# Optimization experiments

Hardware: AMD Instinct MI355X
Metric: run time of the kernel (lower is better)

Reference implementation:

```python
import jax, jax.numpy as jnp
import numpy as np

N_NODES = 100000
N_EDGES = 1250000
D_FEAT = 64
K = 10          # propagation steps (hardcoded in module)
ALPHA = 0.1     # teleport probability (hardcoded in module)


def setup_inputs() -> dict:
    key = jax.random.key(0)
    k1, k2 = jax.random.split(key)
    x = jax.random.normal(k1, (N_NODES, D_FEAT), dtype=jnp.float32)
    # edge_index[0] = source nodes (j), edge_index[1] = target nodes (i)
    edge_index = jax.random.randint(k2, (2, N_EDGES), 0, N_NODES, dtype=jnp.int32)
    return {"x": x, "edge_index": edge_index}


def reference(x, edge_index):
    # PyG APPNP with add_self_loops=False, dropout=0:
    #   gcn_norm: deg[i] = sum of unit edge weights into i (scatter on col)
    #   norm_e = deg^{-1/2}[row_e] * deg^{-1/2}[col_e]
    #   h_{k+1} = (1 - alpha) * A_hat h_k + alpha * x
    row, col = edge_index[0], edge_index[1]
    ones = jnp.ones((edge_index.shape[1],), dtype=x.dtype)
    deg = jax.ops.segment_sum(ones, col, num_segments=N_NODES)
    dinv_sqrt = jnp.where(deg > 0, jax.lax.rsqrt(jnp.where(deg > 0, deg, 1.0)), 0.0)
    norm = dinv_sqrt[row] * dinv_sqrt[col]  # [E]

    h = x
    for _ in range(K):
        # gather-scale-scatter: messages norm_e * h[src_e], aggregated at dst_e
        msg = norm[:, None] * h[row]                           # [E, D]
        agg = jax.ops.segment_sum(msg, col, num_segments=N_NODES)  # [N, D]
        h = (1.0 - ALPHA) * agg + ALPHA * x
    return h
```

## Files before the change

kernel.cpp:

```cpp
#include <hip/hip_runtime.h>

constexpr int DFEAT  = 64;
constexpr int KSTEPS = 10;
constexpr float ALPHA = 0.1f;
constexpr int PAD    = 4;

constexpr int SCAN_T    = 256;
constexpr int SCAN_I    = 4;
constexpr int SCAN_TILE = SCAN_T * SCAN_I;

typedef unsigned int u32;
typedef __attribute__((ext_vector_type(4))) unsigned int u32x4;

__device__ inline u32 f2bf(float f) {
    u32 u = __float_as_uint(f);
    return ((u + 0x7fffu + ((u >> 16) & 1u)) >> 16) & 0xFFFFu;
}
__device__ inline float bfLO(u32 v) { return __uint_as_float(v << 16); }
__device__ inline float bfHI(u32 v) { return __uint_as_float(v & 0xFFFF0000u); }

__global__ void k_hist(const int* __restrict__ col, int* __restrict__ deg, int E) {
    int stride = gridDim.x * blockDim.x;
    for (int e = blockIdx.x * blockDim.x + threadIdx.x; e < E; e += stride)
        atomicAdd(&deg[col[e]], 1);
}

__global__ void k_dinv(const int* __restrict__ deg, float* __restrict__ dinv,
                       int* __restrict__ dpad, int N) {
    int stride = gridDim.x * blockDim.x;
    for (int i = blockIdx.x * blockDim.x + threadIdx.x; i < N; i += stride) {
        int d = deg[i];
        dinv[i] = (d > 0) ? rsqrtf((float)d) : 0.0f;
        dpad[i] = (d + (PAD - 1)) & ~(PAD - 1);
    }
}

__global__ void k_scan1(const int* __restrict__ in, int* __restrict__ out,
                        int* __restrict__ bsum, int n) {
    __shared__ int s[SCAN_T];
    int tid  = threadIdx.x;
    int base = blockIdx.x * SCAN_TILE + tid * SCAN_I;
    int v[SCAN_I];
    int sum = 0;
#pragma unroll
    for (int j = 0; j < SCAN_I; ++j) {
        v[j] = (base + j < n) ? in[base + j] : 0;
        sum += v[j];
    }
    s[tid] = sum;
    __syncthreads();
    for (int ofs = 1; ofs < SCAN_T; ofs <<= 1) {
        int t = (tid >= ofs) ? s[tid - ofs] : 0;
        __syncthreads();
        s[tid] += t;
        __syncthreads();
    }
    int excl = (tid == 0) ? 0 : s[tid - 1];
    if (tid == SCAN_T - 1) bsum[blockIdx.x] = s[tid];
#pragma unroll
    for (int j = 0; j < SCAN_I; ++j) {
        if (base + j < n) out[base + j] = excl;
        excl += v[j];
    }
}

__global__ void k_scan2(int* __restrict__ bsum, int nb) {
    if (threadIdx.x == 0 && blockIdx.x == 0) {
        int acc = 0;
        for (int i = 0; i < nb; ++i) { int t = bsum[i]; bsum[i] = acc; acc += t; }
    }
}

__global__ void k_scan3(int* __restrict__ offs, int* __restrict__ cursor,
                        const int* __restrict__ bsum, int n) {
    int add  = bsum[blockIdx.x];
    int base = blockIdx.x * SCAN_TILE + threadIdx.x * SCAN_I;
#pragma unroll
    for (int j = 0; j < SCAN_I; ++j) {
        int i = base + j;
        if (i < n) { int o = offs[i] + add; offs[i] = o; cursor[i] = o; }
    }
}

__global__ void k_fill(const int* __restrict__ row, const int* __restrict__ col,
                       const float* __restrict__ dinv, int* __restrict__ cursor,
                       u32* __restrict__ meta, int E) {
    int stride = gridDim.x * blockDim.x;
    for (int e = blockIdx.x * blockDim.x + threadIdx.x; e < E; e += stride) {
        int r = row[e], c = col[e];
        int pos = atomicAdd(&cursor[c], 1);
        float w = dinv[r] * dinv[c];
        u32 wq = (u32)__float2int_rn(w * 32768.0f);
        if (wq > 32767u) wq = 32767u;
        __builtin_nontemporal_store((wq << 17) | (u32)r, &meta[pos]);
    }
}

__global__ void k_cvt(const float* __restrict__ x, u32* __restrict__ xb, int n8) {
    int stride = gridDim.x * blockDim.x;
    const float4* x4 = (const float4*)x;
    u32x4* o4 = (u32x4*)xb;
    for (int i = blockIdx.x * blockDim.x + threadIdx.x; i < n8; i += stride) {
        float4 a = x4[2 * i], b = x4[2 * i + 1];
        u32x4 o;
        o.x = (f2bf(a.y) << 16) | f2bf(a.x);
        o.y = (f2bf(a.w) << 16) | f2bf(a.z);
        o.z = (f2bf(b.y) << 16) | f2bf(b.x);
        o.w = (f2bf(b.w) << 16) | f2bf(b.z);
        o4[i] = o;
    }
}

template<bool LAST>
__global__ void __launch_bounds__(256) k_prop(
    const int* __restrict__ offs, const int* __restrict__ dpad,
    const u32* __restrict__ meta, const u32* __restrict__ hsrc,
    const float* __restrict__ x, const u32* __restrict__ xb,
    void* __restrict__ hdst, int N) {
    int gid = (int)((blockIdx.x * blockDim.x + threadIdx.x) >> 3);
    int l   = threadIdx.x & 7;
    if (gid >= N) return;
    int j   = offs[gid];
    int end = j + dpad[gid];

    const u32x4* h4 = (const u32x4*)hsrc;
    float a0 = 0.f, a1 = 0.f, a2 = 0.f, a3 = 0.f,
          a4 = 0.f, a5 = 0.f, a6 = 0.f, a7 = 0.f;

    if (j < end) {
        u32x4 mq = *(const u32x4*)&meta[j];
        while (j < end) {
            int jn = j + 4;
            u32x4 mqn = *(const u32x4*)&meta[jn];
            u32x4 q0 = h4[(size_t)(mq.x & 0x1FFFFu) * 8 + l];
            u32x4 q1 = h4[(size_t)(mq.y & 0x1FFFFu) * 8 + l];
            u32x4 q2 = h4[(size_t)(mq.z & 0x1FFFFu) * 8 + l];
            u32x4 q3 = h4[(size_t)(mq.w & 0x1FFFFu) * 8 + l];
            float w0 = (float)(mq.x >> 17) * (1.0f / 32768.0f);
            float w1 = (float)(mq.y >> 17) * (1.0f / 32768.0f);
            float w2 = (float)(mq.z >> 17) * (1.0f / 32768.0f);
            float w3 = (float)(mq.w >> 17) * (1.0f / 32768.0f);
            a0 += w0 * bfLO(q0.x); a1 += w0 * bfHI(q0.x);
            a2 += w0 * bfLO(q0.y); a3 += w0 * bfHI(q0.y);
            a4 += w0 * bfLO(q0.z); a5 += w0 * bfHI(q0.z);
            a6 += w0 * bfLO(q0.w); a7 += w0 * bfHI(q0.w);
            a0 += w1 * bfLO(q1.x); a1 += w1 * bfHI(q1.x);
            a2 += w1 * bfLO(q1.y); a3 += w1 * bfHI(q1.y);
            a4 += w1 * bfLO(q1.z); a5 += w1 * bfHI(q1.z);
            a6 += w1 * bfLO(q1.w); a7 += w1 * bfHI(q1.w);
            a0 += w2 * bfLO(q2.x); a1 += w2 * bfHI(q2.x);
            a2 += w2 * bfLO(q2.y); a3 += w2 * bfHI(q2.y);
            a4 += w2 * bfLO(q2.z); a5 += w2 * bfHI(q2.z);
            a6 += w2 * bfLO(q2.w); a7 += w2 * bfHI(q2.w);
            a0 += w3 * bfLO(q3.x); a1 += w3 * bfHI(q3.x);
            a2 += w3 * bfLO(q3.y); a3 += w3 * bfHI(q3.y);
            a4 += w3 * bfLO(q3.z); a5 += w3 * bfHI(q3.z);
            a6 += w3 * bfLO(q3.w); a7 += w3 * bfHI(q3.w);
            mq = mqn; j = jn;
        }
    }

    if (LAST) {
        size_t base = (size_t)gid * DFEAT + (size_t)l * 8;
        float4 xa = *(const float4*)&x[base];
        float4 xc = *(const float4*)&x[base + 4];
        float r0 = (1.0f - ALPHA) * a0 + ALPHA * xa.x;
        float r1 = (1.0f - ALPHA) * a1 + ALPHA * xa.y;
        float r2 = (1.0f - ALPHA) * a2 + ALPHA * xa.z;
        float r3 = (1.0f - ALPHA) * a3 + ALPHA * xa.w;
        float r4 = (1.0f - ALPHA) * a4 + ALPHA * xc.x;
        float r5 = (1.0f - ALPHA) * a5 + ALPHA * xc.y;
        float r6 = (1.0f - ALPHA) * a6 + ALPHA * xc.z;
        float r7 = (1.0f - ALPHA) * a7 + ALPHA * xc.w;
        float* o = (float*)hdst;
        *(float4*)&o[base]     = make_float4(r0, r1, r2, r3);
        *(float4*)&o[base + 4] = make_float4(r4, r5, r6, r7);
    } else {
        u32x4 t = ((const u32x4*)xb)[(size_t)gid * 8 + l];
        float r0 = (1.0f - ALPHA) * a0 + ALPHA * bfLO(t.x);
        float r1 = (1.0f - ALPHA) * a1 + ALPHA * bfHI(t.x);
        float r2 = (1.0f - ALPHA) * a2 + ALPHA * bfLO(t.y);
        float r3 = (1.0f - ALPHA) * a3 + ALPHA * bfHI(t.y);
        float r4 = (1.0f - ALPHA) * a4 + ALPHA * bfLO(t.z);
        float r5 = (1.0f - ALPHA) * a5 + ALPHA * bfHI(t.z);
        float r6 = (1.0f - ALPHA) * a6 + ALPHA * bfLO(t.w);
        float r7 = (1.0f - ALPHA) * a7 + ALPHA * bfHI(t.w);
        u32x4 o;
        o.x = (f2bf(r1) << 16) | f2bf(r0);
        o.y = (f2bf(r3) << 16) | f2bf(r2);
        o.z = (f2bf(r5) << 16) | f2bf(r4);
        o.w = (f2bf(r7) << 16) | f2bf(r6);
        ((u32x4*)hdst)[(size_t)gid * 8 + l] = o;
    }
}

extern "C" void kernel_launch(void* const* d_in, const int* in_sizes, int n_in,
                              void* d_out, int out_size, void* d_ws, size_t ws_size,
                              hipStream_t stream) {
    const float* x  = (const float*)d_in[0];
    const int*   ei = (const int*)d_in[1];
    const int N = in_sizes[0] / DFEAT;
    const int E = in_sizes[1] / 2;
    const int* row = ei;
    const int* col = ei + E;

    char* ws = (char*)d_ws;
    auto align256 = [](size_t v) { return (v + 255) & ~(size_t)255; };
    size_t off = 0;
    int* deg = (int*)(ws + off);        off += align256((size_t)N * 4);
    int* dpad = (int*)(ws + off);       off += align256((size_t)N * 4);
    float* dinv = (float*)(ws + off);   off += align256((size_t)N * 4);
    int* offs = (int*)(ws + off);       off += align256((size_t)N * 4);
    int* cursor = (int*)(ws + off);     off += align256((size_t)N * 4);
    int* bsum = (int*)(ws + off);       off += align256((size_t)4096);
    size_t metaCap = (size_t)E + (size_t)(PAD - 1) * N + 16;
    u32* meta = (u32*)(ws + off);       off += align256(metaCap * 4);
    u32* xb = (u32*)(ws + off);         off += align256((size_t)N * 32 * 4);
    u32* hA = (u32*)(ws + off);         off += align256((size_t)N * 32 * 4);
    u32* hB = (u32*)(ws + off);         off += align256((size_t)N * 32 * 4);

    float* out = (float*)d_out;

    const int BLK = 256;
    const int gridE = (E + BLK - 1) / BLK;
    const int gridN = (N + BLK - 1) / BLK;
    const int nb    = (N + SCAN_TILE - 1) / SCAN_TILE;
    const int n8    = N * DFEAT / 8;
    const int gridC = (n8 + BLK - 1) / BLK;
    const int gridProp = (N * 8 + BLK - 1) / BLK;

    hipMemsetAsync(deg, 0, (size_t)N * 4, stream);
    hipMemsetAsync(meta, 0, metaCap * 4, stream);
    k_hist <<<gridE, BLK, 0, stream>>>(col, deg, E);
    k_dinv <<<gridN, BLK, 0, stream>>>(deg, dinv, dpad, N);
    k_scan1<<<nb, SCAN_T, 0, stream>>>(dpad, offs, bsum, N);
    k_scan2<<<1, 64, 0, stream>>>(bsum, nb);
    k_scan3<<<nb, SCAN_T, 0, stream>>>(offs, cursor, bsum, N);
    k_fill <<<gridE, BLK, 0, stream>>>(row, col, dinv, cursor, meta, E);
    k_cvt  <<<gridC, BLK, 0, stream>>>(x, xb, n8);

    u32* bufs[2] = { hA, hB };
    for (int k = 0; k < KSTEPS; ++k) {
        const u32* src = (k == 0) ? xb : bufs[(k + 1) & 1];
        if (k < KSTEPS - 1) {
            k_prop<false><<<gridProp, BLK, 0, stream>>>(offs, dpad, meta, src, x, xb,
                                                        (void*)bufs[k & 1], N);
        } else {
            k_prop<true><<<gridProp, BLK, 0, stream>>>(offs, dpad, meta, src, x, xb,
                                                       (void*)out, N);
        }
    }
    (void)ws_size; (void)n_in; (void)out_size;
}
```

Baseline: 417.5 us.

## Replace global-atomic CSR fill with two-pass bucketed counting sort

The per-edge global atomic scatter into the CSR is replaced by a two-level counting sort. Edges are first partitioned into coarse buckets of 256 destination nodes, using shared-memory histograms and one global atomic per bucket per block. Each bucket is then filled by one block using LDS cursors and cached dinv values. The aim is to cut contention from scattered global atomics and random writes during CSR construction. The cost is an extra E-sized intermediate buffer, an extra pass, and several small kernel launches. The bucketed code also assumes N/256 is at most 512 and that the row index fits in 24 bits.

```diff
diff --git a/kernel.cpp b/kernel.cpp
--- a/kernel.cpp
+++ b/kernel.cpp
@@ -4,6 +4,8 @@
 constexpr int KSTEPS = 10;
 constexpr float ALPHA = 0.1f;
 constexpr int PAD    = 4;
+constexpr int BSHIFT = 8;
+constexpr int MAXBUCK = 512;
 
 constexpr int SCAN_T    = 256;
 constexpr int SCAN_I    = 4;
@@ -71,28 +73,88 @@
     }
 }
 
-__global__ void k_scan3(int* __restrict__ offs, int* __restrict__ cursor,
-                        const int* __restrict__ bsum, int n) {
+__global__ void k_scan3(int* __restrict__ offs, const int* __restrict__ bsum, int n) {
     int add  = bsum[blockIdx.x];
     int base = blockIdx.x * SCAN_TILE + threadIdx.x * SCAN_I;
 #pragma unroll
     for (int j = 0; j < SCAN_I; ++j) {
         int i = base + j;
-        if (i < n) { int o = offs[i] + add; offs[i] = o; cursor[i] = o; }
-    }
-}
-
-__global__ void k_fill(const int* __restrict__ row, const int* __restrict__ col,
-                       const float* __restrict__ dinv, int* __restrict__ cursor,
-                       u32* __restrict__ meta, int E) {
-    int stride = gridDim.x * blockDim.x;
-    for (int e = blockIdx.x * blockDim.x + threadIdx.x; e < E; e += stride) {
-        int r = row[e], c = col[e];
-        int pos = atomicAdd(&cursor[c], 1);
-        float w = dinv[r] * dinv[c];
+        if (i < n) offs[i] += add;
+    }
+}
+
+__global__ void k_bsum(const int* __restrict__ deg, int* __restrict__ btotal, int N) {
+    __shared__ int red[256];
+    int b = blockIdx.x, t = threadIdx.x;
+    int node = (b << BSHIFT) + t;
+    red[t] = (node < N) ? deg[node] : 0;
+    __syncthreads();
+    for (int o = 128; o > 0; o >>= 1) {
+        if (t < o) red[t] += red[t + o];
+        __syncthreads();
+    }
+    if (t == 0) btotal[b] = red[0];
+}
+
+__global__ void k_bscan(const int* __restrict__ btotal, int* __restrict__ bstart,
+                        int* __restrict__ bcur, int nb) {
+    __shared__ int s[MAXBUCK];
+    int t = threadIdx.x;
+    if (t < nb) s[t] = btotal[t];
+    __syncthreads();
+    if (t == 0) {
+        int acc = 0;
+        for (int i = 0; i < nb; ++i) { int v = s[i]; s[i] = acc; acc += v; }
+    }
+    __syncthreads();
+    if (t < nb) { bstart[t] = s[t]; bcur[t * 16] = s[t]; }
+}
+
+__global__ void __launch_bounds__(256) k_bucketA(
+    const int* __restrict__ row, const int* __restrict__ col,
+    int* __restrict__ bcur, u32* __restrict__ bucketed,
+    int E, int nb, int chunk) {
+    __shared__ int hist[MAXBUCK];
+    __shared__ int cur[MAXBUCK];
+    int t  = threadIdx.x;
+    int e0 = blockIdx.x * chunk;
+    int e1 = min(E, e0 + chunk);
+    for (int b = t; b < nb; b += 256) hist[b] = 0;
+    __syncthreads();
+    for (int e = e0 + t; e < e1; e += 256)
+        atomicAdd(&hist[col[e] >> BSHIFT], 1);
+    __syncthreads();
+    for (int b = t; b < nb; b += 256)
+        cur[b] = hist[b] ? atomicAdd(&bcur[b * 16], hist[b]) : 0;
+    __syncthreads();
+    for (int e = e0 + t; e < e1; e += 256) {
+        int c = col[e], r = row[e];
+        int rank = atomicAdd(&cur[c >> BSHIFT], 1);
+        bucketed[rank] = ((u32)r << BSHIFT) | (u32)(c & ((1 << BSHIFT) - 1));
+    }
+}
+
+__global__ void __launch_bounds__(256) k_fillB(
+    const u32* __restrict__ bucketed, const int* __restrict__ bstart,
+    const int* __restrict__ btotal, const int* __restrict__ offs,
+    const float* __restrict__ dinv, u32* __restrict__ meta, int N) {
+    __shared__ int   lcur[256];
+    __shared__ float ldinv[256];
+    int b = blockIdx.x, t = threadIdx.x;
+    int node = (b << BSHIFT) + t;
+    lcur[t]  = (node < N) ? offs[node] : 0;
+    ldinv[t] = (node < N) ? dinv[node] : 0.0f;
+    __syncthreads();
+    int p0 = bstart[b], p1 = p0 + btotal[b];
+    for (int p = p0 + t; p < p1; p += 256) {
+        u32 v  = bucketed[p];
+        int r  = (int)(v >> BSHIFT);
+        int cl = (int)(v & 255u);
+        int pos = atomicAdd(&lcur[cl], 1);
+        float w = dinv[r] * ldinv[cl];
         u32 wq = (u32)__float2int_rn(w * 32768.0f);
         if (wq > 32767u) wq = 32767u;
-        __builtin_nontemporal_store((wq << 17) | (u32)r, &meta[pos]);
+        meta[pos] = (wq << 17) | (u32)r;
     }
 }
 
@@ -204,6 +266,8 @@
     const int* row = ei;
     const int* col = ei + E;
 
+    const int NBUCK = (N + ((1 << BSHIFT) - 1)) >> BSHIFT;
+
     char* ws = (char*)d_ws;
     auto align256 = [](size_t v) { return (v + 255) & ~(size_t)255; };
     size_t off = 0;
@@ -211,8 +275,11 @@
     int* dpad = (int*)(ws + off);       off += align256((size_t)N * 4);
     float* dinv = (float*)(ws + off);   off += align256((size_t)N * 4);
     int* offs = (int*)(ws + off);       off += align256((size_t)N * 4);
-    int* cursor = (int*)(ws + off);     off += align256((size_t)N * 4);
     int* bsum = (int*)(ws + off);       off += align256((size_t)4096);
+    int* btotal = (int*)(ws + off);     off += align256((size_t)MAXBUCK * 4);
+    int* bstart = (int*)(ws + off);     off += align256((size_t)MAXBUCK * 4);
+    int* bcur = (int*)(ws + off);       off += align256((size_t)MAXBUCK * 64);
+    u32* bucketed = (u32*)(ws + off);   off += align256((size_t)E * 4);
     size_t metaCap = (size_t)E + (size_t)(PAD - 1) * N + 16;
     u32* meta = (u32*)(ws + off);       off += align256(metaCap * 4);
     u32* xb = (u32*)(ws + off);         off += align256((size_t)N * 32 * 4);
@@ -228,6 +295,8 @@
     const int n8    = N * DFEAT / 8;
     const int gridC = (n8 + BLK - 1) / BLK;
     const int gridProp = (N * 8 + BLK - 1) / BLK;
+    const int GR_A = 128;
+    const int chunkA = (E + GR_A - 1) / GR_A;
 
     hipMemsetAsync(deg, 0, (size_t)N * 4, stream);
     hipMemsetAsync(meta, 0, metaCap * 4, stream);
@@ -235,8 +304,11 @@
     k_dinv <<<gridN, BLK, 0, stream>>>(deg, dinv, dpad, N);
     k_scan1<<<nb, SCAN_T, 0, stream>>>(dpad, offs, bsum, N);
     k_scan2<<<1, 64, 0, stream>>>(bsum, nb);
-    k_scan3<<<nb, SCAN_T, 0, stream>>>(offs, cursor, bsum, N);
-    k_fill <<<gridE, BLK, 0, stream>>>(row, col, dinv, cursor, meta, E);
+    k_scan3<<<nb, SCAN_T, 0, stream>>>(offs, bsum, N);
+    k_bsum <<<NBUCK, 256, 0, stream>>>(deg, btotal, N);
+    k_bscan<<<1, MAXBUCK, 0, stream>>>(btotal, bstart, bcur, NBUCK);
+    k_bucketA<<<GR_A, BLK, 0, stream>>>(row, col, bcur, bucketed, E, NBUCK, chunkA);
+    k_fillB<<<NBUCK, BLK, 0, stream>>>(bucketed, bstart, btotal, offs, dinv, meta, N);
     k_cvt  <<<gridC, BLK, 0, stream>>>(x, xb, n8);
 
     u32* bufs[2] = { hA, hB };
```

Result: faster. 393.5 us (-5.7%).
